# Performance work log

Hardware: AMD Instinct MI355X
Metric: run time of the kernel (lower is better)

## Reference

```python
import jax, jax.numpy as jnp
import numpy as np

B_ = 2; S_ = 2048; H_ = 2048; NH = 16; HD = H_ // NH; BS = 256
SCALE = 1.0 / np.sqrt(HD).astype(np.float32)

def setup_inputs() -> dict:
    key = jax.random.key(0)
    ks = jax.random.split(key, 5)
    return {
        'hidden_states': jax.random.normal(ks[0], (B_, S_, H_), dtype=jnp.float32),
        'Wq': jax.random.normal(ks[1], (H_, H_), dtype=jnp.float32) * 0.02,
        'Wk': jax.random.normal(ks[2], (H_, H_), dtype=jnp.float32) * 0.02,
        'Wv': jax.random.normal(ks[3], (H_, H_), dtype=jnp.float32) * 0.02,
        'Wo': jax.random.normal(ks[4], (H_, H_), dtype=jnp.float32) * 0.02,
    }

def _split_heads(x):
    b, s, _ = x.shape
    return x.reshape(b, s, NH, HD).transpose(0, 2, 1, 3)  # [b,h,s,d]

def _attn(q, k, v):
    # Faithful to the module's per-block softmax (NOT true online-softmax):
    # each kv block j<=i gets an independent softmax over its bs keys; the
    # block outputs are summed and divided by the sum of all attention weights.
    b, h, s, d = q.shape
    nb = s // BS
    kb = k.reshape(b, h, nb, BS, d)
    vb = v.reshape(b, h, nb, BS, d)
    scores = jnp.einsum('bhsd,bhjkd->bhsjk', q, kb) * SCALE  # [b,h,S,nb,BS]
    qi = jnp.arange(s)
    bi = qi // BS                                # query block index [S]
    bj = jnp.arange(nb)                          # key block index  [nb]
    kidx = bj[:, None] * BS + jnp.arange(BS)[None, :]  # absolute key idx [nb,BS]
    # causal mask only bites on the diagonal block (j == i)
    diag_mask = (bi[:, None, None] == bj[None, :, None]) & (kidx[None] > qi[:, None, None])
    scores = jnp.where(diag_mask[None, None], -jnp.inf, scores)
    w = jax.nn.softmax(scores.astype(jnp.float32), axis=-1)  # per-block softmax
    include = (bj[None, :] <= bi[:, None]).astype(w.dtype)   # skip blocks j > i
    w = w * include[None, None, :, :, None]
    out = jnp.einsum('bhsjk,bhjkd->bhsd', w, vb)
    norm = jnp.sum(w, axis=(-2, -1), keepdims=False)[..., None]  # [b,h,S,1]
    return out / (norm + 1e-6)

def reference(hidden_states, Wq, Wk, Wv, Wo):
    q = _split_heads(hidden_states @ Wq.T)
    k = _split_heads(hidden_states @ Wk.T)
    v = _split_heads(hidden_states @ Wv.T)
    o = _attn(q, k, v)  # [b,h,s,d]
    b, h, s, d = o.shape
    merged = o.transpose(0, 2, 1, 3).reshape(b, s, h * d)
    return merged @ Wo.T
```

## Files before the change

kernel.cpp:

```cpp
#include <hip/hip_runtime.h>
#include <stdint.h>
#include <stddef.h>

constexpr int B_ = 2;
constexpr int S_ = 2048;
constexpr int H_ = 2048;
constexpr int NH_ = 16;
constexpr int HD_ = 128;
constexpr int BS_ = 256;
constexpr float SCALE_ = 0.08838834764831845f;

typedef __bf16 bf16x8 __attribute__((ext_vector_type(8)));
typedef float floatx4 __attribute__((ext_vector_type(4)));
typedef uint16_t u16x8 __attribute__((ext_vector_type(8)));

static __device__ __forceinline__ bf16x8 ld16(const uint16_t* p) {
    return __builtin_bit_cast(bf16x8, *reinterpret_cast<const uint4*>(p));
}
static __device__ __forceinline__ uint16_t f2b(float f) {
    return __builtin_bit_cast(uint16_t, (__bf16)f);
}

template <bool F32>
static __device__ __forceinline__ uint4 ldrow(const void* base, size_t eoff) {
    if constexpr (F32) {
        const float* p = (const float*)base + eoff;
        const float4 lo = *reinterpret_cast<const float4*>(p);
        const float4 hi = *reinterpret_cast<const float4*>(p + 4);
        u16x8 k;
        k[0] = f2b(lo.x); k[1] = f2b(lo.y); k[2] = f2b(lo.z); k[3] = f2b(lo.w);
        k[4] = f2b(hi.x); k[5] = f2b(hi.y); k[6] = f2b(hi.z); k[7] = f2b(hi.w);
        return __builtin_bit_cast(uint4, k);
    } else {
        return *reinterpret_cast<const uint4*>((const uint16_t*)base + eoff);
    }
}

static __device__ __forceinline__ void gld_lds16(const uint16_t* g, const uint4* lds_wave_base) {
    __builtin_amdgcn_global_load_lds(
        (const __attribute__((address_space(1))) uint32_t*)g,
        (__attribute__((address_space(3))) uint32_t*)lds_wave_base,
        16, 0, 0);
}

__global__ __launch_bounds__(256) void cvt_kernel(const float* __restrict__ src,
                                                  uint16_t* __restrict__ dst) {
    const size_t i = (size_t)blockIdx.x * 256 + threadIdx.x;
    reinterpret_cast<uint4*>(dst)[i] = ldrow<true>(src, i * 8);
}

template <bool TSTORE, bool OF32, bool WBF16>
__global__ __launch_bounds__(256, 2) void gemm_bt(const uint16_t* __restrict__ A,
                                                  const void* __restrict__ W,
                                                  void* __restrict__ C) {
    constexpr int K = H_;
    constexpr int N = H_;
    __shared__ uint4 As[1024];
    __shared__ uint4 Bs[1024];

    const int tid = threadIdx.x;
    const int lane = tid & 63;
    const int wave = tid >> 6;
    const int col = lane & 15;
    const int quad = lane >> 4;
    const int m0 = blockIdx.y * 128;
    const int n0 = blockIdx.x * 128;
    const int wr = (wave >> 1) * 64;
    const int wc = (wave & 1) * 64;

    const uint16_t* Abase = A + (size_t)m0 * K;
    const uint16_t* Wb16 = (const uint16_t*)W + (WBF16 ? (size_t)n0 * K : 0);

    floatx4 acc[4][4] = {};

    for (int kb = 0; kb < K; kb += 64) {
        if constexpr (WBF16) {
            __syncthreads();
#pragma unroll
            for (int i = 0; i < 4; ++i) {
                const int L = tid + i * 256;
                const int row = L >> 3;
                const int gch = (L & 7) ^ (row & 7);
                gld_lds16(Abase + (size_t)row * K + kb + gch * 8, &As[i * 256 + wave * 64]);
                gld_lds16(Wb16 + (size_t)row * K + kb + gch * 8, &Bs[i * 256 + wave * 64]);
            }
            __syncthreads();
        } else {
            uint4 bv[4];
#pragma unroll
            for (int i = 0; i < 4; ++i) {
                const int L = tid + i * 256;
                const int row = L >> 3;
                const int gch = (L & 7) ^ (row & 7);
                bv[i] = ldrow<true>(W, (size_t)n0 * K + (size_t)row * K + kb + gch * 8);
            }
            __syncthreads();
#pragma unroll
            for (int i = 0; i < 4; ++i) {
                const int L = tid + i * 256;
                const int row = L >> 3;
                const int gch = (L & 7) ^ (row & 7);
                gld_lds16(Abase + (size_t)row * K + kb + gch * 8, &As[i * 256 + wave * 64]);
            }
#pragma unroll
            for (int i = 0; i < 4; ++i) Bs[tid + i * 256] = bv[i];
            __syncthreads();
        }
#pragma unroll
        for (int ks = 0; ks < 2; ++ks) {
            bf16x8 af[4], bfr[4];
            const int ch = ks * 4 + quad;
#pragma unroll
            for (int mt = 0; mt < 4; ++mt) {
                const int m = wr + mt * 16 + col;
                af[mt] = __builtin_bit_cast(bf16x8, As[m * 8 + (ch ^ (m & 7))]);
            }
#pragma unroll
            for (int nt = 0; nt < 4; ++nt) {
                const int n = wc + nt * 16 + col;
                bfr[nt] = __builtin_bit_cast(bf16x8, Bs[n * 8 + (ch ^ (n & 7))]);
            }
#pragma unroll
            for (int mt = 0; mt < 4; ++mt)
#pragma unroll
                for (int nt = 0; nt < 4; ++nt)
                    acc[mt][nt] = __builtin_amdgcn_mfma_f32_16x16x32_bf16(
                        af[mt], bfr[nt], acc[mt][nt], 0, 0, 0);
        }
    }

#pragma unroll
    for (int mt = 0; mt < 4; ++mt) {
#pragma unroll
        for (int nt = 0; nt < 4; ++nt) {
#pragma unroll
            for (int r = 0; r < 4; ++r) {
                const int row = m0 + wr + mt * 16 + quad * 4 + r;
                const int cc = n0 + wc + nt * 16 + col;
                const float v = acc[mt][nt][r];
                if constexpr (OF32) {
                    ((float*)C)[(size_t)row * N + cc] = v;
                } else if constexpr (!TSTORE) {
                    ((uint16_t*)C)[(size_t)row * N + cc] = f2b(v);
                } else {
                    const int b = row >> 11;
                    const int s = row & (S_ - 1);
                    const int h = cc >> 7;
                    const int d = cc & (HD_ - 1);
                    ((uint16_t*)C)[((size_t)((b * NH_ + h) * HD_ + d) << 11) + s] = f2b(v);
                }
            }
        }
    }
}

__global__ __launch_bounds__(256, 2) void attn_kernel(const uint16_t* __restrict__ Q,
                                                      const uint16_t* __restrict__ Kp,
                                                      const uint16_t* __restrict__ Vt,
                                                      uint16_t* __restrict__ O) {
    __shared__ uint4 Stg[2048];
    __shared__ uint4 Pl[4 * 16 * 33];
    const int tid = threadIdx.x;
    const int lane = tid & 63;
    const int wave = tid >> 6;
    const int col = lane & 15;
    const int quad = lane >> 4;
    const int b = blockIdx.z;
    const int h = blockIdx.y;
    const int p = blockIdx.x;

    const uint16_t* Qb = Q + (size_t)b * S_ * H_ + h * HD_;
    const uint16_t* Kb = Kp + (size_t)b * S_ * H_ + h * HD_;
    const uint16_t* Vb = Vt + (size_t)(b * NH_ + h) * HD_ * S_;
    uint16_t* Ob = O + (size_t)b * S_ * H_ + h * HD_;

    uint16_t* Pw = reinterpret_cast<uint16_t*>(Pl) + wave * 16 * 264;
    const uint4* Pr = Pl + wave * (16 * 33) + col * 33;

#pragma unroll
    for (int ti = 0; ti < 2; ++ti) {
        const int t = ti ? (31 - p) : p;
        const int bi = t >> 2;
        const int q0 = t * 64 + wave * 16;

        bf16x8 aq[4];
#pragma unroll
        for (int ks = 0; ks < 4; ++ks)
            aq[ks] = ld16(Qb + (size_t)(q0 + col) * H_ + ks * 32 + quad * 8);

        floatx4 o[8] = {};

        for (int j = 0; j <= bi; ++j) {
            floatx4 s[16];
#pragma unroll
            for (int half = 0; half < 2; ++half) {
                __syncthreads();
                const uint16_t* src = Kb + (size_t)(j * BS_ + half * 128) * H_;
#pragma unroll
                for (int i = 0; i < 8; ++i) {
                    const int L = tid + i * 256;
                    const int row = L >> 4;
                    const int gc = (L & 15) ^ (row & 15);
                    gld_lds16(src + (size_t)row * H_ + gc * 8, &Stg[i * 256 + wave * 64]);
                }
                __syncthreads();
#pragma unroll
                for (int nt8 = 0; nt8 < 8; ++nt8) {
                    const int n = nt8 * 16 + col;
                    floatx4 a = {};
#pragma unroll
                    for (int ks = 0; ks < 4; ++ks) {
                        const bf16x8 kf = __builtin_bit_cast(
                            bf16x8, Stg[n * 16 + ((ks * 4 + quad) ^ (n & 15))]);
                        a = __builtin_amdgcn_mfma_f32_16x16x32_bf16(aq[ks], kf, a, 0, 0, 0);
                    }
                    s[half * 8 + nt8] = a * SCALE_;
                }
            }
            if (j == bi) {
                const int qq = (q0 & (BS_ - 1)) + quad * 4;
#pragma unroll
                for (int nt = 0; nt < 16; ++nt) {
                    const int key = nt * 16 + col;
#pragma unroll
                    for (int r = 0; r < 4; ++r)
                        if (key > qq + r) s[nt][r] = -1e30f;
                }
            }
#pragma unroll
            for (int r = 0; r < 4; ++r) {
                float sm = 0.f;
#pragma unroll
                for (int nt = 0; nt < 16; ++nt) {
                    const float pw = __expf(s[nt][r]);
                    s[nt][r] = pw;
                    sm += pw;
                }
#pragma unroll
                for (int d = 1; d < 16; d <<= 1) sm += __shfl_xor(sm, d);
                const float inv = 1.0f / sm;
                const int rowoff = (quad * 4 + r) * 264;
#pragma unroll
                for (int nt = 0; nt < 16; ++nt)
                    Pw[rowoff + nt * 16 + col] = f2b(s[nt][r] * inv);
            }
#pragma unroll
            for (int half = 0; half < 2; ++half) {
                __syncthreads();
                const uint16_t* src = Vb + j * BS_ + half * 128;
#pragma unroll
                for (int i = 0; i < 8; ++i) {
                    const int L = tid + i * 256;
                    const int row = L >> 4;
                    const int gc = (L & 15) ^ (row & 15);
                    gld_lds16(src + (size_t)row * S_ + gc * 8, &Stg[i * 256 + wave * 64]);
                }
                __syncthreads();
#pragma unroll
                for (int k4 = 0; k4 < 4; ++k4) {
                    const bf16x8 pa =
                        __builtin_bit_cast(bf16x8, Pr[(half * 4 + k4) * 4 + quad]);
#pragma unroll
                    for (int nd = 0; nd < 8; ++nd) {
                        const int n = nd * 16 + col;
                        const bf16x8 vf = __builtin_bit_cast(
                            bf16x8, Stg[n * 16 + ((k4 * 4 + quad) ^ (n & 15))]);
                        o[nd] = __builtin_amdgcn_mfma_f32_16x16x32_bf16(pa, vf, o[nd], 0, 0, 0);
                    }
                }
            }
        }

        const float rn = 1.0f / ((float)(bi + 1) + 1e-6f);
#pragma unroll
        for (int nd = 0; nd < 8; ++nd)
#pragma unroll
            for (int r = 0; r < 4; ++r)
                Ob[(size_t)(q0 + quad * 4 + r) * H_ + nd * 16 + col] = f2b(o[nd][r] * rn);
    }
}

extern "C" void kernel_launch(void* const* d_in, const int* in_sizes, int n_in,
                              void* d_out, int out_size, void* d_ws, size_t ws_size,
                              hipStream_t stream) {
    const float* X = (const float*)d_in[0];
    const float* Wq = (const float*)d_in[1];
    const float* Wk = (const float*)d_in[2];
    const float* Wv = (const float*)d_in[3];
    const float* Wo = (const float*)d_in[4];

    const size_t elems = (size_t)B_ * S_ * H_;
    const size_t welems = (size_t)H_ * H_;
    uint16_t* Xb = (uint16_t*)d_ws;
    uint16_t* Qb = Xb + elems;
    uint16_t* Kb = Qb + elems;
    uint16_t* Vt = Kb + elems;
    uint16_t* Ob = Xb;
    uint16_t* Wqb = Vt + elems;
    uint16_t* Wkb = Wqb + welems;
    uint16_t* Wvb = Wkb + welems;
    uint16_t* Wob = Wvb + welems;

    const bool bigws = ws_size >= (size_t)96 * 1024 * 1024;

    cvt_kernel<<<(int)(elems / 8 / 256), 256, 0, stream>>>(X, Xb);

    dim3 gg(H_ / 128, (B_ * S_) / 128);
    dim3 ga(16, NH_, B_);

    if (bigws) {
        const int wgrid = (int)(welems / 8 / 256);
        cvt_kernel<<<wgrid, 256, 0, stream>>>(Wq, Wqb);
        cvt_kernel<<<wgrid, 256, 0, stream>>>(Wk, Wkb);
        cvt_kernel<<<wgrid, 256, 0, stream>>>(Wv, Wvb);
        cvt_kernel<<<wgrid, 256, 0, stream>>>(Wo, Wob);
        gemm_bt<false, false, true><<<gg, 256, 0, stream>>>(Xb, Wqb, Qb);
        gemm_bt<false, false, true><<<gg, 256, 0, stream>>>(Xb, Wkb, Kb);
        gemm_bt<true, false, true><<<gg, 256, 0, stream>>>(Xb, Wvb, Vt);
        attn_kernel<<<ga, 256, 0, stream>>>(Qb, Kb, Vt, Ob);
        gemm_bt<false, true, true><<<gg, 256, 0, stream>>>(Ob, Wob, d_out);
    } else {
        gemm_bt<false, false, false><<<gg, 256, 0, stream>>>(Xb, Wq, Qb);
        gemm_bt<false, false, false><<<gg, 256, 0, stream>>>(Xb, Wk, Kb);
        gemm_bt<true, false, false><<<gg, 256, 0, stream>>>(Xb, Wv, Vt);
        attn_kernel<<<ga, 256, 0, stream>>>(Qb, Kb, Vt, Ob);
        gemm_bt<false, true, false><<<gg, 256, 0, stream>>>(Ob, Wo, d_out);
    }
}
```

Before: 385.1 us.

## Batch weight conversions and QKV GEMMs into single launches, remap attention grid per XCD

Combines the four weight fp32-to-bf16 conversions into one launch, and merges the Q/K/V projection GEMMs into one 3D-grid launch. This cuts launch overhead and lets the three GEMMs share the whole GPU at once, giving a larger wave of blocks. The attention grid is flattened to 1D and remapped so each XCD gets contiguous (batch, head) groups, aiming for better L2 locality of K/V. The fp32-weight fallback path is split into its own kernel; it keeps its old logic, with the new grid mapping.

```diff
diff --git a/kernel.cpp b/kernel.cpp
--- a/kernel.cpp
+++ b/kernel.cpp
@@ -49,63 +49,49 @@
     reinterpret_cast<uint4*>(dst)[i] = ldrow<true>(src, i * 8);
 }
 
-template <bool TSTORE, bool OF32, bool WBF16>
-__global__ __launch_bounds__(256, 2) void gemm_bt(const uint16_t* __restrict__ A,
-                                                  const void* __restrict__ W,
-                                                  void* __restrict__ C) {
+__global__ __launch_bounds__(256) void cvt4_kernel(const float* __restrict__ s0,
+                                                   const float* __restrict__ s1,
+                                                   const float* __restrict__ s2,
+                                                   const float* __restrict__ s3,
+                                                   uint16_t* __restrict__ d0,
+                                                   uint16_t* __restrict__ d1,
+                                                   uint16_t* __restrict__ d2,
+                                                   uint16_t* __restrict__ d3) {
+    const int w = blockIdx.y;
+    const float* src = (w == 0) ? s0 : (w == 1) ? s1 : (w == 2) ? s2 : s3;
+    uint16_t* dst = (w == 0) ? d0 : (w == 1) ? d1 : (w == 2) ? d2 : d3;
+    const size_t i = (size_t)blockIdx.x * 256 + threadIdx.x;
+    reinterpret_cast<uint4*>(dst)[i] = ldrow<true>(src, i * 8);
+}
+
+template <bool TSTORE, bool OF32>
+static __device__ __forceinline__ void gemm_body(const uint16_t* __restrict__ Abase,
+                                                 const uint16_t* __restrict__ Wbase,
+                                                 void* __restrict__ C,
+                                                 int m0, int n0, uint4* As, uint4* Bs) {
     constexpr int K = H_;
     constexpr int N = H_;
-    __shared__ uint4 As[1024];
-    __shared__ uint4 Bs[1024];
-
     const int tid = threadIdx.x;
     const int lane = tid & 63;
     const int wave = tid >> 6;
     const int col = lane & 15;
     const int quad = lane >> 4;
-    const int m0 = blockIdx.y * 128;
-    const int n0 = blockIdx.x * 128;
     const int wr = (wave >> 1) * 64;
     const int wc = (wave & 1) * 64;
 
-    const uint16_t* Abase = A + (size_t)m0 * K;
-    const uint16_t* Wb16 = (const uint16_t*)W + (WBF16 ? (size_t)n0 * K : 0);
-
     floatx4 acc[4][4] = {};
 
     for (int kb = 0; kb < K; kb += 64) {
-        if constexpr (WBF16) {
-            __syncthreads();
-#pragma unroll
-            for (int i = 0; i < 4; ++i) {
-                const int L = tid + i * 256;
-                const int row = L >> 3;
-                const int gch = (L & 7) ^ (row & 7);
-                gld_lds16(Abase + (size_t)row * K + kb + gch * 8, &As[i * 256 + wave * 64]);
-                gld_lds16(Wb16 + (size_t)row * K + kb + gch * 8, &Bs[i * 256 + wave * 64]);
-            }
-            __syncthreads();
-        } else {
-            uint4 bv[4];
-#pragma unroll
-            for (int i = 0; i < 4; ++i) {
-                const int L = tid + i * 256;
-                const int row = L >> 3;
-                const int gch = (L & 7) ^ (row & 7);
-                bv[i] = ldrow<true>(W, (size_t)n0 * K + (size_t)row * K + kb + gch * 8);
-            }
-            __syncthreads();
-#pragma unroll
-            for (int i = 0; i < 4; ++i) {
-                const int L = tid + i * 256;
-                const int row = L >> 3;
-                const int gch = (L & 7) ^ (row & 7);
-                gld_lds16(Abase + (size_t)row * K + kb + gch * 8, &As[i * 256 + wave * 64]);
-            }
-#pragma unroll
-            for (int i = 0; i < 4; ++i) Bs[tid + i * 256] = bv[i];
-            __syncthreads();
-        }
+        __syncthreads();
+#pragma unroll
+        for (int i = 0; i < 4; ++i) {
+            const int L = tid + i * 256;
+            const int row = L >> 3;
+            const int gch = (L & 7) ^ (row & 7);
+            gld_lds16(Abase + (size_t)row * K + kb + gch * 8, &As[i * 256 + wave * 64]);
+            gld_lds16(Wbase + (size_t)row * K + kb + gch * 8, &Bs[i * 256 + wave * 64]);
+        }
+        __syncthreads();
 #pragma unroll
         for (int ks = 0; ks < 2; ++ks) {
             bf16x8 af[4], bfr[4];
@@ -154,6 +140,123 @@
     }
 }
 
+template <bool TSTORE, bool OF32>
+__global__ __launch_bounds__(256, 2) void gemm_bt(const uint16_t* __restrict__ A,
+                                                  const uint16_t* __restrict__ W,
+                                                  void* __restrict__ C) {
+    __shared__ uint4 As[1024];
+    __shared__ uint4 Bs[1024];
+    const int m0 = blockIdx.y * 128;
+    const int n0 = blockIdx.x * 128;
+    gemm_body<TSTORE, OF32>(A + (size_t)m0 * H_, W + (size_t)n0 * H_, C, m0, n0, As, Bs);
+}
+
+__global__ __launch_bounds__(256, 2) void gemm_qkv(const uint16_t* __restrict__ A,
+                                                   const uint16_t* __restrict__ Wq,
+                                                   const uint16_t* __restrict__ Wk,
+                                                   const uint16_t* __restrict__ Wv,
+                                                   uint16_t* __restrict__ Qb,
+                                                   uint16_t* __restrict__ Kb,
+                                                   uint16_t* __restrict__ Vt) {
+    __shared__ uint4 As[1024];
+    __shared__ uint4 Bs[1024];
+    const int z = blockIdx.z;
+    const int m0 = blockIdx.y * 128;
+    const int n0 = blockIdx.x * 128;
+    const uint16_t* W = (z == 0) ? Wq : (z == 1) ? Wk : Wv;
+    const uint16_t* Ab = A + (size_t)m0 * H_;
+    const uint16_t* Wb = W + (size_t)n0 * H_;
+    if (z == 2)
+        gemm_body<true, false>(Ab, Wb, Vt, m0, n0, As, Bs);
+    else
+        gemm_body<false, false>(Ab, Wb, (z == 0) ? Qb : Kb, m0, n0, As, Bs);
+}
+
+template <bool TSTORE, bool OF32>
+__global__ __launch_bounds__(256, 2) void gemm_bt_f32w(const uint16_t* __restrict__ A,
+                                                       const float* __restrict__ W,
+                                                       void* __restrict__ C) {
+    constexpr int K = H_;
+    constexpr int N = H_;
+    __shared__ uint4 As[1024];
+    __shared__ uint4 Bs[1024];
+    const int tid = threadIdx.x;
+    const int lane = tid & 63;
+    const int wave = tid >> 6;
+    const int col = lane & 15;
+    const int quad = lane >> 4;
+    const int m0 = blockIdx.y * 128;
+    const int n0 = blockIdx.x * 128;
+    const int wr = (wave >> 1) * 64;
+    const int wc = (wave & 1) * 64;
+    const uint16_t* Abase = A + (size_t)m0 * K;
+
+    floatx4 acc[4][4] = {};
+    for (int kb = 0; kb < K; kb += 64) {
+        uint4 bv[4];
+#pragma unroll
+        for (int i = 0; i < 4; ++i) {
+            const int L = tid + i * 256;
+            const int row = L >> 3;
+            const int gch = (L & 7) ^ (row & 7);
+            bv[i] = ldrow<true>(W, (size_t)n0 * K + (size_t)row * K + kb + gch * 8);
+        }
+        __syncthreads();
+#pragma unroll
+        for (int i = 0; i < 4; ++i) {
+            const int L = tid + i * 256;
+            const int row = L >> 3;
+            const int gch = (L & 7) ^ (row & 7);
+            gld_lds16(Abase + (size_t)row * K + kb + gch * 8, &As[i * 256 + wave * 64]);
+        }
+#pragma unroll
+        for (int i = 0; i < 4; ++i) Bs[tid + i * 256] = bv[i];
+        __syncthreads();
+#pragma unroll
+        for (int ks = 0; ks < 2; ++ks) {
+            bf16x8 af[4], bfr[4];
+            const int ch = ks * 4 + quad;
+#pragma unroll
+            for (int mt = 0; mt < 4; ++mt) {
+                const int m = wr + mt * 16 + col;
+                af[mt] = __builtin_bit_cast(bf16x8, As[m * 8 + (ch ^ (m & 7))]);
+            }
+#pragma unroll
+            for (int nt = 0; nt < 4; ++nt) {
+                const int n = wc + nt * 16 + col;
+                bfr[nt] = __builtin_bit_cast(bf16x8, Bs[n * 8 + (ch ^ (n & 7))]);
+            }
+#pragma unroll
+            for (int mt = 0; mt < 4; ++mt)
+#pragma unroll
+                for (int nt = 0; nt < 4; ++nt)
+                    acc[mt][nt] = __builtin_amdgcn_mfma_f32_16x16x32_bf16(
+                        af[mt], bfr[nt], acc[mt][nt], 0, 0, 0);
+        }
+    }
+#pragma unroll
+    for (int mt = 0; mt < 4; ++mt)
+#pragma unroll
+        for (int nt = 0; nt < 4; ++nt)
+#pragma unroll
+            for (int r = 0; r < 4; ++r) {
+                const int row = m0 + wr + mt * 16 + quad * 4 + r;
+                const int cc = n0 + wc + nt * 16 + col;
+                const float v = acc[mt][nt][r];
+                if constexpr (OF32) {
+                    ((float*)C)[(size_t)row * N + cc] = v;
+                } else if constexpr (!TSTORE) {
+                    ((uint16_t*)C)[(size_t)row * N + cc] = f2b(v);
+                } else {
+                    const int b = row >> 11;
+                    const int s = row & (S_ - 1);
+                    const int h = cc >> 7;
+                    const int d = cc & (HD_ - 1);
+                    ((uint16_t*)C)[((size_t)((b * NH_ + h) * HD_ + d) << 11) + s] = f2b(v);
+                }
+            }
+}
+
 __global__ __launch_bounds__(256, 2) void attn_kernel(const uint16_t* __restrict__ Q,
                                                       const uint16_t* __restrict__ Kp,
                                                       const uint16_t* __restrict__ Vt,
@@ -165,9 +268,14 @@
     const int wave = tid >> 6;
     const int col = lane & 15;
     const int quad = lane >> 4;
-    const int b = blockIdx.z;
-    const int h = blockIdx.y;
-    const int p = blockIdx.x;
+
+    const int id = blockIdx.x;
+    const int xcd = id & 7;
+    const int slot = id >> 3;
+    const int grp = xcd * 4 + (slot >> 4);
+    const int p = slot & 15;
+    const int b = grp >> 4;
+    const int h = grp & 15;
 
     const uint16_t* Qb = Q + (size_t)b * S_ * H_ + h * HD_;
     const uint16_t* Kb = Kp + (size_t)b * S_ * H_ + h * HD_;
@@ -306,24 +414,19 @@
     cvt_kernel<<<(int)(elems / 8 / 256), 256, 0, stream>>>(X, Xb);
 
     dim3 gg(H_ / 128, (B_ * S_) / 128);
-    dim3 ga(16, NH_, B_);
 
     if (bigws) {
-        const int wgrid = (int)(welems / 8 / 256);
-        cvt_kernel<<<wgrid, 256, 0, stream>>>(Wq, Wqb);
-        cvt_kernel<<<wgrid, 256, 0, stream>>>(Wk, Wkb);
-        cvt_kernel<<<wgrid, 256, 0, stream>>>(Wv, Wvb);
-        cvt_kernel<<<wgrid, 256, 0, stream>>>(Wo, Wob);
-        gemm_bt<false, false, true><<<gg, 256, 0, stream>>>(Xb, Wqb, Qb);
-        gemm_bt<false, false, true><<<gg, 256, 0, stream>>>(Xb, Wkb, Kb);
-        gemm_bt<true, false, true><<<gg, 256, 0, stream>>>(Xb, Wvb, Vt);
-        attn_kernel<<<ga, 256, 0, stream>>>(Qb, Kb, Vt, Ob);
-        gemm_bt<false, true, true><<<gg, 256, 0, stream>>>(Ob, Wob, d_out);
+        dim3 gw((int)(welems / 8 / 256), 4);
+        cvt4_kernel<<<gw, 256, 0, stream>>>(Wq, Wk, Wv, Wo, Wqb, Wkb, Wvb, Wob);
+        dim3 gqkv(H_ / 128, (B_ * S_) / 128, 3);
+        gemm_qkv<<<gqkv, 256, 0, stream>>>(Xb, Wqb, Wkb, Wvb, Qb, Kb, Vt);
+        attn_kernel<<<512, 256, 0, stream>>>(Qb, Kb, Vt, Ob);
+        gemm_bt<false, true><<<gg, 256, 0, stream>>>(Ob, Wob, d_out);
     } else {
-        gemm_bt<false, false, false><<<gg, 256, 0, stream>>>(Xb, Wq, Qb);
-        gemm_bt<false, false, false><<<gg, 256, 0, stream>>>(Xb, Wk, Kb);
-        gemm_bt<true, false, false><<<gg, 256, 0, stream>>>(Xb, Wv, Vt);
-        attn_kernel<<<ga, 256, 0, stream>>>(Qb, Kb, Vt, Ob);
-        gemm_bt<false, true, false><<<gg, 256, 0, stream>>>(Ob, Wo, d_out);
-    }
-}
+        gemm_bt_f32w<false, false><<<gg, 256, 0, stream>>>(Xb, Wq, Qb);
+        gemm_bt_f32w<false, false><<<gg, 256, 0, stream>>>(Xb, Wk, Kb);
+        gemm_bt_f32w<true, false><<<gg, 256, 0, stream>>>(Xb, Wv, Vt);
+        attn_kernel<<<512, 256, 0, stream>>>(Qb, Kb, Vt, Ob);
+        gemm_bt_f32w<false, true><<<gg, 256, 0, stream>>>(Ob, Wo, d_out);
+    }
+}
```

Result: faster. 352.8 us (-8.4%).
